# Kernel tuning notes

Measured on AMD Instinct MI355X. Metric: run time of the kernel, lower is better.

## Reference

```python
import jax, jax.numpy as jnp
import numpy as np
from jax import lax

DILATIONS = [1, 2, 4, 8, 16, 32, 64, 128, 256, 512]
KERNEL = 3
CH = 64
B, T = 8, 16384
L = len(DILATIONS)


def setup_inputs() -> dict:
    key = jax.random.key(0)
    ks = jax.random.split(key, 5)
    x = jax.random.normal(ks[0], (B, CH, T), dtype=jnp.float32)
    # gated conv: out_channels = 2*CH (tanh half | sigmoid half)
    weights_conv = jax.random.normal(ks[1], (L, 2 * CH, CH, KERNEL), dtype=jnp.float32) * 0.1
    biases_conv = jax.random.normal(ks[2], (L, 2 * CH), dtype=jnp.float32) * 0.1
    weights_out = jax.random.normal(ks[3], (L, CH, CH), dtype=jnp.float32) * 0.1
    biases_out = jax.random.normal(ks[4], (L, CH), dtype=jnp.float32) * 0.1
    return {
        "x": x,
        "weights_conv": weights_conv,
        "biases_conv": biases_conv,
        "weights_out": weights_out,
        "biases_out": biases_out,
    }


def _stack_forward(x, weights_conv, biases_conv, weights_out, biases_out):
    skips = []
    for i, d in enumerate(DILATIONS):
        h = x  # residual branch
        pad = (KERNEL - 1) * d  # causal left padding
        y = lax.conv_general_dilated(
            x, weights_conv[i],
            window_strides=(1,), padding=[(pad, 0)], rhs_dilation=(d,),
            dimension_numbers=("NCH", "OIH", "NCH"),
        ) + biases_conv[i][None, :, None]
        yt, ys = jnp.split(y, 2, axis=1)          # gated activation
        a = jnp.tanh(yt) * jax.nn.sigmoid(ys)      # (B, CH, T)
        skips.append(a)                            # skip = activation output
        if i < L - 1:  # last layer has use_output_transform=False
            out = jnp.einsum("oc,bct->bot", weights_out[i], a) + biases_out[i][None, :, None]
        else:
            out = a
        x = out + h  # residual add
    # pack (output, skips[0..L-1]) into one array of shape (L+1, B, CH, T)
    return jnp.concatenate([x[None], jnp.stack(skips, axis=0)], axis=0)


def reference(x, weights_conv, biases_conv, weights_out, biases_out):
    return _stack_forward(x, weights_conv, biases_conv, weights_out, biases_out)
```

## Files before the change

### kernel.cpp

```cpp
#include <hip/hip_runtime.h>
#include <hip/hip_bf16.h>


#define CH 64
#define TLEN 16384
#define NB 8
#define BN 128
#define NLAYER 10

#define WP   192
#define PSTR 194
#define ASTR 130

typedef __attribute__((ext_vector_type(4))) float f32x4;
typedef __attribute__((ext_vector_type(8))) short s16x8;
typedef __attribute__((ext_vector_type(4))) unsigned short u16x4;

__device__ __forceinline__ unsigned short f2bf(float f) {
    union { float f; unsigned u; } v; v.f = f;
    unsigned r = v.u + 0x7fffu + ((v.u >> 16) & 1u);
    return (unsigned short)(r >> 16);
}
__device__ __forceinline__ float bf2f(unsigned short u) {
    union { unsigned u; float f; } v; v.u = ((unsigned)u) << 16;
    return v.f;
}
__device__ __forceinline__ void gload_lds16(const void* g, void* l) {
    __builtin_amdgcn_global_load_lds(
        (const __attribute__((address_space(1))) unsigned int*)g,
        (__attribute__((address_space(3))) unsigned int*)l, 16, 0, 0);
}

#define NCONV (NLAYER * 4 * 2 * 6 * 64 * 8)
#define NOUT  (NLAYER * 4 * 2 * 64 * 8)

__global__ void pack_weights(const float* __restrict__ wconv,
                             const float* __restrict__ wout,
                             unsigned short* __restrict__ wcpk,
                             unsigned short* __restrict__ wopk)
{
    int idx = blockIdx.x * 256 + threadIdx.x;
    if (idx < NCONV) {
        int j = idx & 7, t = idx >> 3;
        int lane = t & 63; t >>= 6;
        int ks = t % 6;   t /= 6;
        int m  = t & 1;   t >>= 1;
        int wv = t & 3;   int l = t >> 2;
        int o  = (m * 4 + wv) * 16 + (lane & 15);
        int ck = ks * 32 + (lane >> 4) * 8 + j;
        int kk = ck >> 6, c = ck & 63;
        wcpk[idx] = f2bf(wconv[(((size_t)l * 128 + o) * CH + c) * 3 + (2 - kk)]);
    } else if (idx < NCONV + NOUT) {
        int id = idx - NCONV;
        int j = id & 7, t = id >> 3;
        int lane = t & 63; t >>= 6;
        int ks = t & 1;    t >>= 1;
        int wv = t & 3;    int l = t >> 2;
        int o  = wv * 16 + (lane & 15);
        int c  = ks * 32 + (lane >> 4) * 8 + j;
        wopk[id] = f2bf(wout[((size_t)l * CH + o) * CH + c]);
    }
}

__global__ __launch_bounds__(256, 2)
void wavenet_head(const float* __restrict__ x, unsigned short* __restrict__ xplane,
                  float* __restrict__ out,
                  const unsigned short* __restrict__ wcpk,
                  const unsigned short* __restrict__ wopk,
                  const float* __restrict__ bconv, const float* __restrict__ bout)
{
    __shared__ __align__(16) unsigned short pl[2][8 * PSTR * 8];
    __shared__ __align__(16) unsigned short as_[8 * ASTR * 8];

    const int tid  = threadIdx.x;
    const int lane = tid & 63;
    const int wv   = tid >> 6;
    const int hrow = lane & 15;
    const int kgrp = lane >> 4;
    const int b  = blockIdx.y;
    const int t0 = blockIdx.x * BN;
    const size_t xbase  = (size_t)b * CH * TLEN;
    const size_t planeF = (size_t)NB * CH * TLEN;

    if (tid < WP) {
        const int tt = t0 - 64 + tid;
        #pragma unroll
        for (int c8 = 0; c8 < 8; ++c8) {
            s16x8 pk = {0, 0, 0, 0, 0, 0, 0, 0};
            if (tt >= 0) {
                const float* p = x + xbase + (size_t)(c8 * 8) * TLEN + tt;
                #pragma unroll
                for (int j = 0; j < 8; ++j) pk[j] = (short)f2bf(p[(size_t)j * TLEN]);
            }
            *reinterpret_cast<s16x8*>(&pl[0][(size_t)(c8 * PSTR + tid) * 8]) = pk;
        }
    }
    __syncthreads();

    int cur = 0;
    for (int l = 0; l < 5; ++l) {
        const int dil = 1 << l;
        unsigned short* plc = pl[cur];
        unsigned short* pln = pl[cur ^ 1];

        s16x8 wa[2][6];
        {
            const unsigned short* basew = wcpk + ((size_t)(l * 4 + wv) * 768 + lane) * 8;
            #pragma unroll
            for (int m = 0; m < 2; ++m)
                #pragma unroll
                for (int ks = 0; ks < 6; ++ks)
                    wa[m][ks] = *reinterpret_cast<const s16x8*>(basew + (size_t)(m * 6 + ks) * 512);
        }
        const float* Bc = bconv + (size_t)l * 128;
        float bt[4], bs[4];
        #pragma unroll
        for (int r = 0; r < 4; ++r) {
            bt[r] = Bc[wv * 16 + kgrp * 4 + r];
            bs[r] = Bc[64 + wv * 16 + kgrp * 4 + r];
        }
        s16x8 wa2[2];
        {
            const unsigned short* b2 = wopk + ((size_t)(l * 4 + wv) * 128 + lane) * 8;
            wa2[0] = *reinterpret_cast<const s16x8*>(b2);
            wa2[1] = *reinterpret_cast<const s16x8*>(b2 + 512);
        }
        const float* Bo = bout + (size_t)l * CH;
        float bo[4];
        #pragma unroll
        for (int r = 0; r < 4; ++r) bo[r] = Bo[wv * 16 + kgrp * 4 + r];

        f32x4 accT[12], accS[12];
        #pragma unroll
        for (int nt = 0; nt < 12; ++nt) {
            accT[nt] = (f32x4){0.f, 0.f, 0.f, 0.f};
            accS[nt] = (f32x4){0.f, 0.f, 0.f, 0.f};
        }
        #pragma unroll
        for (int nt = 0; nt < 12; ++nt) {
            #pragma unroll
            for (int ks = 0; ks < 6; ++ks) {
                const int kb = ks * 4 + kgrp;
                const int kk = kb >> 3, c8i = kb & 7;
                int q = nt * 16 + hrow - kk * dil;
                if (q < 0) q = 0;
                const s16x8 bf = *reinterpret_cast<const s16x8*>(&plc[(size_t)(c8i * PSTR + q) * 8]);
                accT[nt] = __builtin_amdgcn_mfma_f32_16x16x32_bf16(wa[0][ks], bf, accT[nt], 0, 0, 0);
                accS[nt] = __builtin_amdgcn_mfma_f32_16x16x32_bf16(wa[1][ks], bf, accS[nt], 0, 0, 0);
            }
        }

        float* skipl = out + (size_t)(1 + l) * planeF + xbase;
        const int o0 = wv * 16 + kgrp * 4;

        #pragma unroll
        for (int nt = 0; nt < 8; ++nt) {
            #pragma unroll
            for (int r = 0; r < 4; ++r) {
                const float yt = accT[nt][r] + bt[r];
                const float ys = accS[nt][r] + bs[r];
                const float th = 2.f * __builtin_amdgcn_rcpf(1.f + __expf(-2.f * yt)) - 1.f;
                const float sg = __builtin_amdgcn_rcpf(1.f + __expf(-ys));
                const float av = th * sg;
                const int c = wv * 16 + kgrp * 4 + r;
                const int p = nt * 16 + hrow;
                if (nt >= 4) skipl[(size_t)c * TLEN + t0 + p - 64] = av;
                as_[(size_t)((c >> 3) * ASTR + p) * 8 + (c & 7)] = f2bf(av);
            }
        }
        __syncthreads();
        #pragma unroll
        for (int nt = 0; nt < 8; ++nt) {
            f32x4 a2 = (f32x4){0.f, 0.f, 0.f, 0.f};
            const int p = nt * 16 + hrow;
            #pragma unroll
            for (int ks2 = 0; ks2 < 2; ++ks2) {
                const s16x8 bf = *reinterpret_cast<const s16x8*>(
                    &as_[(size_t)((ks2 * 4 + kgrp) * ASTR + p) * 8]);
                a2 = __builtin_amdgcn_mfma_f32_16x16x32_bf16(wa2[ks2], bf, a2, 0, 0, 0);
            }
            const int tt = t0 - 64 + p;
            const u16x4 rv = *reinterpret_cast<const u16x4*>(
                &plc[(size_t)((o0 >> 3) * PSTR + p) * 8 + (o0 & 7)]);
            if (l == 4) {
                if (nt >= 4) {
                    u16x4 ov;
                    #pragma unroll
                    for (int r = 0; r < 4; ++r) ov[r] = f2bf(a2[r] + bo[r] + bf2f(rv[r]));
                    *reinterpret_cast<u16x4*>(&xplane[xbase + (size_t)tt * CH + o0]) = ov;
                }
            } else {
                u16x4 ov;
                #pragma unroll
                for (int r = 0; r < 4; ++r)
                    ov[r] = (tt >= 0) ? f2bf(a2[r] + bo[r] + bf2f(rv[r])) : (unsigned short)0;
                *reinterpret_cast<u16x4*>(&pln[(size_t)((o0 >> 3) * PSTR + p) * 8 + (o0 & 7)]) = ov;
            }
        }
        __syncthreads();
        #pragma unroll
        for (int nt = 8; nt < 12; ++nt) {
            #pragma unroll
            for (int r = 0; r < 4; ++r) {
                const float yt = accT[nt][r] + bt[r];
                const float ys = accS[nt][r] + bs[r];
                const float th = 2.f * __builtin_amdgcn_rcpf(1.f + __expf(-2.f * yt)) - 1.f;
                const float sg = __builtin_amdgcn_rcpf(1.f + __expf(-ys));
                const float av = th * sg;
                const int c = wv * 16 + kgrp * 4 + r;
                const int p = nt * 16 + hrow;
                skipl[(size_t)c * TLEN + t0 + p - 64] = av;
                as_[(size_t)((c >> 3) * ASTR + p - 128) * 8 + (c & 7)] = f2bf(av);
            }
        }
        __syncthreads();
        #pragma unroll
        for (int nt = 8; nt < 12; ++nt) {
            f32x4 a2 = (f32x4){0.f, 0.f, 0.f, 0.f};
            const int p = nt * 16 + hrow;
            #pragma unroll
            for (int ks2 = 0; ks2 < 2; ++ks2) {
                const s16x8 bf = *reinterpret_cast<const s16x8*>(
                    &as_[(size_t)((ks2 * 4 + kgrp) * ASTR + p - 128) * 8]);
                a2 = __builtin_amdgcn_mfma_f32_16x16x32_bf16(wa2[ks2], bf, a2, 0, 0, 0);
            }
            const int tt = t0 - 64 + p;
            const u16x4 rv = *reinterpret_cast<const u16x4*>(
                &plc[(size_t)((o0 >> 3) * PSTR + p) * 8 + (o0 & 7)]);
            if (l == 4) {
                u16x4 ov;
                #pragma unroll
                for (int r = 0; r < 4; ++r) ov[r] = f2bf(a2[r] + bo[r] + bf2f(rv[r]));
                *reinterpret_cast<u16x4*>(&xplane[xbase + (size_t)tt * CH + o0]) = ov;
            } else {
                u16x4 ov;
                #pragma unroll
                for (int r = 0; r < 4; ++r) ov[r] = f2bf(a2[r] + bo[r] + bf2f(rv[r]));
                *reinterpret_cast<u16x4*>(&pln[(size_t)((o0 >> 3) * PSTR + p) * 8 + (o0 & 7)]) = ov;
            }
        }
        __syncthreads();

        cur ^= 1;
    }
}

template<int SM, bool LAST>
__global__ __launch_bounds__(256, 3)
void wavenet_layer(const void* __restrict__ xin_, void* __restrict__ xout_,
                   float* __restrict__ skip,
                   const unsigned short* __restrict__ wcpk,
                   const unsigned short* __restrict__ wopk,
                   const float* __restrict__ bconv, const float* __restrict__ bout,
                   int layer, int dil)
{
    extern __shared__ __align__(16) unsigned short xs[];
    unsigned short* as_ = xs;

    const int tid  = threadIdx.x;
    const int lane = tid & 63;
    const int wv   = tid >> 6;
    const int hrow = lane & 15;
    const int kgrp = lane >> 4;
    const int b  = blockIdx.y;
    const int t0 = blockIdx.x * BN;
    const int NW = BN + 2 * dil;
    const size_t xbase = (size_t)b * CH * TLEN;

    if (SM == 1) {
        const unsigned short* xin = (const unsigned short*)xin_;
        const int cnt_n = (NW + 63) >> 6;
        if (t0 >= 2 * dil) {
            for (int ch = wv; ch < 8 * cnt_n; ch += 4) {
                const int c8 = ch / cnt_n;
                const int n0 = (ch % cnt_n) * 64;
                const int rem = NW - n0;
                const unsigned short* src =
                    xin + xbase + (size_t)(t0 - 2 * dil + n0 + lane) * CH + c8 * 8;
                unsigned short* dst = &xs[(size_t)(c8 * NW + n0) * 8];
                if (rem >= 64) gload_lds16(src, dst);
                else if (lane < rem) gload_lds16(src, dst);
            }
        } else {
            for (int ch = wv; ch < 8 * cnt_n; ch += 4) {
                const int c8 = ch / cnt_n;
                const int n0 = (ch % cnt_n) * 64;
                if (n0 + lane < NW) {
                    const int tg = t0 - 2 * dil + n0 + lane;
                    s16x8 pk = {0, 0, 0, 0, 0, 0, 0, 0};
                    if (tg >= 0)
                        pk = *reinterpret_cast<const s16x8*>(xin + xbase + (size_t)tg * CH + c8 * 8);
                    *reinterpret_cast<s16x8*>(&xs[(size_t)(c8 * NW + n0 + lane) * 8]) = pk;
                }
            }
        }
    } else {
        const unsigned short* xin = (const unsigned short*)xin_;
        if (t0 >= 2 * dil) {
            for (int ch = wv; ch < 48; ch += 4) {
                const int kk = ch >> 4, c8 = (ch >> 1) & 7, n0 = (ch & 1) * 64;
                const unsigned short* src =
                    xin + xbase + (size_t)(t0 + n0 + lane - kk * dil) * CH + c8 * 8;
                unsigned short* dst = &xs[(size_t)((kk * 8 + c8) * BN + n0) * 8];
                gload_lds16(src, dst);
            }
        } else {
            for (int ch = wv; ch < 48; ch += 4) {
                const int kk = ch >> 4, c8 = (ch >> 1) & 7, n0 = (ch & 1) * 64;
                const int tg = t0 + n0 + lane - kk * dil;
                s16x8 pk = {0, 0, 0, 0, 0, 0, 0, 0};
                if (tg >= 0)
                    pk = *reinterpret_cast<const s16x8*>(xin + xbase + (size_t)tg * CH + c8 * 8);
                *reinterpret_cast<s16x8*>(&xs[(size_t)((kk * 8 + c8) * BN + n0 + lane) * 8]) = pk;
            }
        }
    }

    s16x8 wa[2][6];
    {
        const unsigned short* base = wcpk + ((size_t)(layer * 4 + wv) * 768 + lane) * 8;
        #pragma unroll
        for (int m = 0; m < 2; ++m)
            #pragma unroll
            for (int ks = 0; ks < 6; ++ks)
                wa[m][ks] = *reinterpret_cast<const s16x8*>(base + (size_t)(m * 6 + ks) * 512);
    }
    const float* Bc = bconv + (size_t)layer * 128;
    float bt[4], bs[4];
    #pragma unroll
    for (int r = 0; r < 4; ++r) {
        bt[r] = Bc[wv * 16 + kgrp * 4 + r];
        bs[r] = Bc[64 + wv * 16 + kgrp * 4 + r];
    }

    __syncthreads();

    f32x4 accT[8], accS[8];
    #pragma unroll
    for (int nt = 0; nt < 8; ++nt) {
        accT[nt] = (f32x4){0.f, 0.f, 0.f, 0.f};
        accS[nt] = (f32x4){0.f, 0.f, 0.f, 0.f};
    }
    #pragma unroll
    for (int nt = 0; nt < 8; ++nt) {
        #pragma unroll
        for (int ks = 0; ks < 6; ++ks) {
            const int kb = ks * 4 + kgrp;
            const unsigned short* bp;
            if (SM == 2) {
                bp = &xs[(size_t)(kb * BN + nt * 16 + hrow) * 8];
            } else {
                const int kk = kb >> 3, c8i = kb & 7;
                bp = &xs[(size_t)(c8i * NW + nt * 16 + hrow + (2 - kk) * dil) * 8];
            }
            const s16x8 bf = *reinterpret_cast<const s16x8*>(bp);
            accT[nt] = __builtin_amdgcn_mfma_f32_16x16x32_bf16(wa[0][ks], bf, accT[nt], 0, 0, 0);
            accS[nt] = __builtin_amdgcn_mfma_f32_16x16x32_bf16(wa[1][ks], bf, accS[nt], 0, 0, 0);
        }
    }

    if (!LAST) __syncthreads();

    #pragma unroll
    for (int nt = 0; nt < 8; ++nt) {
        #pragma unroll
        for (int r = 0; r < 4; ++r) {
            const float yt = accT[nt][r] + bt[r];
            const float ys = accS[nt][r] + bs[r];
            const float th = 2.f * __builtin_amdgcn_rcpf(1.f + __expf(-2.f * yt)) - 1.f;
            const float sg = __builtin_amdgcn_rcpf(1.f + __expf(-ys));
            const float av = th * sg;
            const int c = wv * 16 + kgrp * 4 + r;
            const int n = nt * 16 + hrow;
            skip[xbase + (size_t)c * TLEN + t0 + n] = av;
            if (LAST) {
                const float res = bf2f(xs[(size_t)((c >> 3) * BN + n) * 8 + (c & 7)]);
                ((float*)xout_)[xbase + (size_t)c * TLEN + t0 + n] = av + res;
            } else {
                as_[(size_t)((c >> 3) * BN + n) * 8 + (c & 7)] = f2bf(av);
            }
        }
    }

    if (LAST) return;

    __syncthreads();

    const unsigned short* b2 = wopk + ((size_t)(layer * 4 + wv) * 128 + lane) * 8;
    s16x8 wa2[2];
    wa2[0] = *reinterpret_cast<const s16x8*>(b2);
    wa2[1] = *reinterpret_cast<const s16x8*>(b2 + 512);
    const float* Bo = bout + (size_t)layer * CH;
    float bo[4];
    #pragma unroll
    for (int r = 0; r < 4; ++r) bo[r] = Bo[wv * 16 + kgrp * 4 + r];

    const int o0 = wv * 16 + kgrp * 4;
    unsigned short* xout = (unsigned short*)xout_;

    #pragma unroll
    for (int nt = 0; nt < 8; ++nt) {
        f32x4 acc = (f32x4){0.f, 0.f, 0.f, 0.f};
        #pragma unroll
        for (int ks = 0; ks < 2; ++ks) {
            const s16x8 bf = *reinterpret_cast<const s16x8*>(
                &as_[(size_t)((ks * 4 + kgrp) * BN + nt * 16 + hrow) * 8]);
            acc = __builtin_amdgcn_mfma_f32_16x16x32_bf16(wa2[ks], bf, acc, 0, 0, 0);
        }
        const int n = nt * 16 + hrow;
        const u16x4 rv = *reinterpret_cast<const u16x4*>(
            (const unsigned short*)xin_ + xbase + (size_t)(t0 + n) * CH + o0);
        u16x4 ov;
        #pragma unroll
        for (int r = 0; r < 4; ++r) ov[r] = f2bf(acc[r] + bo[r] + bf2f(rv[r]));
        *reinterpret_cast<u16x4*>(&xout[xbase + (size_t)(t0 + n) * CH + o0]) = ov;
    }
}

extern "C" void kernel_launch(void* const* d_in, const int* in_sizes, int n_in,
                              void* d_out, int out_size, void* d_ws, size_t ws_size,
                              hipStream_t stream)
{
    const float* x  = (const float*)d_in[0];
    const float* wc = (const float*)d_in[1];
    const float* bc = (const float*)d_in[2];
    const float* wo = (const float*)d_in[3];
    const float* bo = (const float*)d_in[4];
    float* out = (float*)d_out;
    const size_t planeF  = (size_t)NB * CH * TLEN;
    const size_t planeBy = planeF * sizeof(unsigned short);

    unsigned short* P0 = (unsigned short*)d_ws;
    unsigned short* P1 = (unsigned short*)((char*)d_ws + planeBy);
    unsigned short* wcpk = (unsigned short*)((char*)d_ws + 2 * planeBy);
    unsigned short* wopk = wcpk + NCONV;

    pack_weights<<<(NCONV + NOUT) / 256, 256, 0, stream>>>(wc, wo, wcpk, wopk);

    dim3 grid(TLEN / BN, NB), block(256);

    wavenet_head<<<grid, block, 0, stream>>>(x, P0, out, wcpk, wopk, bc, bo);

    wavenet_layer<1, false><<<grid, block, (size_t)(BN + 64) * 128, stream>>>(
        P0, P1, out + 6 * planeF, wcpk, wopk, bc, bo, 5, 32);
    wavenet_layer<1, false><<<grid, block, (size_t)(BN + 128) * 128, stream>>>(
        P1, P0, out + 7 * planeF, wcpk, wopk, bc, bo, 6, 64);
    wavenet_layer<2, false><<<grid, block, 24 * BN * 8 * 2, stream>>>(
        P0, P1, out + 8 * planeF, wcpk, wopk, bc, bo, 7, 128);
    wavenet_layer<2, false><<<grid, block, 24 * BN * 8 * 2, stream>>>(
        P1, P0, out + 9 * planeF, wcpk, wopk, bc, bo, 8, 256);
    wavenet_layer<2, true><<<grid, block, 24 * BN * 8 * 2, stream>>>(
        P0, out, out + 10 * planeF, wcpk, wopk, bc, bo, 9, 512);
}
```

Measured before the change: 248.2 us.

## Double block to 512 threads, split time tiles across wave halves

```diff
diff --git a/kernel.cpp b/kernel.cpp
--- a/kernel.cpp
+++ b/kernel.cpp
@@ -10,7 +10,7 @@
 
 #define WP   192
 #define PSTR 194
-#define ASTR 130
+#define ASTR 194
 
 typedef __attribute__((ext_vector_type(4))) float f32x4;
 typedef __attribute__((ext_vector_type(8))) short s16x8;
@@ -62,7 +62,7 @@
     }
 }
 
-__global__ __launch_bounds__(256, 2)
+__global__ __launch_bounds__(512, 4)
 void wavenet_head(const float* __restrict__ x, unsigned short* __restrict__ xplane,
                   float* __restrict__ out,
                   const unsigned short* __restrict__ wcpk,
@@ -74,7 +74,9 @@
 
     const int tid  = threadIdx.x;
     const int lane = tid & 63;
-    const int wv   = tid >> 6;
+    const int wv8  = tid >> 6;
+    const int mw   = wv8 & 3;
+    const int nh   = wv8 >> 2;
     const int hrow = lane & 15;
     const int kgrp = lane >> 4;
     const int b  = blockIdx.y;
@@ -82,18 +84,18 @@
     const size_t xbase  = (size_t)b * CH * TLEN;
     const size_t planeF = (size_t)NB * CH * TLEN;
 
-    if (tid < WP) {
-        const int tt = t0 - 64 + tid;
-        #pragma unroll
-        for (int c8 = 0; c8 < 8; ++c8) {
-            s16x8 pk = {0, 0, 0, 0, 0, 0, 0, 0};
-            if (tt >= 0) {
-                const float* p = x + xbase + (size_t)(c8 * 8) * TLEN + tt;
-                #pragma unroll
-                for (int j = 0; j < 8; ++j) pk[j] = (short)f2bf(p[(size_t)j * TLEN]);
-            }
-            *reinterpret_cast<s16x8*>(&pl[0][(size_t)(c8 * PSTR + tid) * 8]) = pk;
-        }
+    #pragma unroll
+    for (int it = 0; it < 3; ++it) {
+        const int q  = it * 512 + tid;
+        const int c8 = q / WP, p = q % WP;
+        const int tt = t0 - 64 + p;
+        s16x8 pk = {0, 0, 0, 0, 0, 0, 0, 0};
+        if (tt >= 0) {
+            const float* pp = x + xbase + (size_t)(c8 * 8) * TLEN + tt;
+            #pragma unroll
+            for (int j = 0; j < 8; ++j) pk[j] = (short)f2bf(pp[(size_t)j * TLEN]);
+        }
+        *reinterpret_cast<s16x8*>(&pl[0][(size_t)(c8 * PSTR + p) * 8]) = pk;
     }
     __syncthreads();
 
@@ -103,76 +105,84 @@
         unsigned short* plc = pl[cur];
         unsigned short* pln = pl[cur ^ 1];
 
-        s16x8 wa[2][6];
+        s16x8 w0[6], w1[6];
         {
-            const unsigned short* basew = wcpk + ((size_t)(l * 4 + wv) * 768 + lane) * 8;
-            #pragma unroll
-            for (int m = 0; m < 2; ++m)
-                #pragma unroll
-                for (int ks = 0; ks < 6; ++ks)
-                    wa[m][ks] = *reinterpret_cast<const s16x8*>(basew + (size_t)(m * 6 + ks) * 512);
+            const unsigned short* basew = wcpk + ((size_t)(l * 4 + mw) * 768 + lane) * 8;
+            #pragma unroll
+            for (int ks = 0; ks < 6; ++ks) {
+                w0[ks] = *reinterpret_cast<const s16x8*>(basew + (size_t)ks * 512);
+                w1[ks] = *reinterpret_cast<const s16x8*>(basew + (size_t)(6 + ks) * 512);
+            }
         }
         const float* Bc = bconv + (size_t)l * 128;
         float bt[4], bs[4];
         #pragma unroll
         for (int r = 0; r < 4; ++r) {
-            bt[r] = Bc[wv * 16 + kgrp * 4 + r];
-            bs[r] = Bc[64 + wv * 16 + kgrp * 4 + r];
-        }
+            bt[r] = Bc[mw * 16 + kgrp * 4 + r];
+            bs[r] = Bc[64 + mw * 16 + kgrp * 4 + r];
+        }
+        float* skipl = out + (size_t)(1 + l) * planeF + xbase;
+
+        #pragma unroll 1
+        for (int hf = 0; hf < 2; ++hf) {
+            f32x4 accT[3], accS[3];
+            #pragma unroll
+            for (int i3 = 0; i3 < 3; ++i3) {
+                accT[i3] = (f32x4){0.f, 0.f, 0.f, 0.f};
+                accS[i3] = (f32x4){0.f, 0.f, 0.f, 0.f};
+            }
+            #pragma unroll
+            for (int i3 = 0; i3 < 3; ++i3) {
+                const int nt = nh * 6 + hf * 3 + i3;
+                const int p  = nt * 16 + hrow;
+                #pragma unroll
+                for (int ks = 0; ks < 6; ++ks) {
+                    const int kb = ks * 4 + kgrp;
+                    const int kk = kb >> 3, c8i = kb & 7;
+                    int q = p - kk * dil;
+                    if (q < 0) q = 0;
+                    const s16x8 bf = *reinterpret_cast<const s16x8*>(
+                        &plc[(size_t)(c8i * PSTR + q) * 8]);
+                    accT[i3] = __builtin_amdgcn_mfma_f32_16x16x32_bf16(w0[ks], bf, accT[i3], 0, 0, 0);
+                    accS[i3] = __builtin_amdgcn_mfma_f32_16x16x32_bf16(w1[ks], bf, accS[i3], 0, 0, 0);
+                }
+            }
+            #pragma unroll
+            for (int i3 = 0; i3 < 3; ++i3) {
+                const int nt = nh * 6 + hf * 3 + i3;
+                const int p  = nt * 16 + hrow;
+                #pragma unroll
+                for (int r = 0; r < 4; ++r) {
+                    const float yt = accT[i3][r] + bt[r];
+                    const float ys = accS[i3][r] + bs[r];
+                    const float th = 2.f * __builtin_amdgcn_rcpf(1.f + __expf(-2.f * yt)) - 1.f;
+                    const float sg = __builtin_amdgcn_rcpf(1.f + __expf(-ys));
+                    const float av = th * sg;
+                    const int c = mw * 16 + kgrp * 4 + r;
+                    if (nt >= 4) skipl[(size_t)c * TLEN + t0 + p - 64] = av;
+                    as_[(size_t)((c >> 3) * ASTR + p) * 8 + (c & 7)] = f2bf(av);
+                }
+            }
+        }
+        __syncthreads();
+
         s16x8 wa2[2];
         {
-            const unsigned short* b2 = wopk + ((size_t)(l * 4 + wv) * 128 + lane) * 8;
+            const unsigned short* b2 = wopk + ((size_t)(l * 4 + mw) * 128 + lane) * 8;
             wa2[0] = *reinterpret_cast<const s16x8*>(b2);
             wa2[1] = *reinterpret_cast<const s16x8*>(b2 + 512);
         }
         const float* Bo = bout + (size_t)l * CH;
         float bo[4];
         #pragma unroll
-        for (int r = 0; r < 4; ++r) bo[r] = Bo[wv * 16 + kgrp * 4 + r];
-
-        f32x4 accT[12], accS[12];
-        #pragma unroll
-        for (int nt = 0; nt < 12; ++nt) {
-            accT[nt] = (f32x4){0.f, 0.f, 0.f, 0.f};
-            accS[nt] = (f32x4){0.f, 0.f, 0.f, 0.f};
-        }
-        #pragma unroll
-        for (int nt = 0; nt < 12; ++nt) {
-            #pragma unroll
-            for (int ks = 0; ks < 6; ++ks) {
-                const int kb = ks * 4 + kgrp;
-                const int kk = kb >> 3, c8i = kb & 7;
-                int q = nt * 16 + hrow - kk * dil;
-                if (q < 0) q = 0;
-                const s16x8 bf = *reinterpret_cast<const s16x8*>(&plc[(size_t)(c8i * PSTR + q) * 8]);
-                accT[nt] = __builtin_amdgcn_mfma_f32_16x16x32_bf16(wa[0][ks], bf, accT[nt], 0, 0, 0);
-                accS[nt] = __builtin_amdgcn_mfma_f32_16x16x32_bf16(wa[1][ks], bf, accS[nt], 0, 0, 0);
-            }
-        }
-
-        float* skipl = out + (size_t)(1 + l) * planeF + xbase;
-        const int o0 = wv * 16 + kgrp * 4;
-
-        #pragma unroll
-        for (int nt = 0; nt < 8; ++nt) {
-            #pragma unroll
-            for (int r = 0; r < 4; ++r) {
-                const float yt = accT[nt][r] + bt[r];
-                const float ys = accS[nt][r] + bs[r];
-                const float th = 2.f * __builtin_amdgcn_rcpf(1.f + __expf(-2.f * yt)) - 1.f;
-                const float sg = __builtin_amdgcn_rcpf(1.f + __expf(-ys));
-                const float av = th * sg;
-                const int c = wv * 16 + kgrp * 4 + r;
-                const int p = nt * 16 + hrow;
-                if (nt >= 4) skipl[(size_t)c * TLEN + t0 + p - 64] = av;
-                as_[(size_t)((c >> 3) * ASTR + p) * 8 + (c & 7)] = f2bf(av);
-            }
-        }
-        __syncthreads();
-        #pragma unroll
-        for (int nt = 0; nt < 8; ++nt) {
+        for (int r = 0; r < 4; ++r) bo[r] = Bo[mw * 16 + kgrp * 4 + r];
+        const int o0 = mw * 16 + kgrp * 4;
+
+        #pragma unroll
+        for (int i = 0; i < 6; ++i) {
+            const int nt = nh * 6 + i;
+            const int p  = nt * 16 + hrow;
             f32x4 a2 = (f32x4){0.f, 0.f, 0.f, 0.f};
-            const int p = nt * 16 + hrow;
             #pragma unroll
             for (int ks2 = 0; ks2 < 2; ++ks2) {
                 const s16x8 bf = *reinterpret_cast<const s16x8*>(
@@ -198,55 +208,13 @@
             }
         }
         __syncthreads();
-        #pragma unroll
-        for (int nt = 8; nt < 12; ++nt) {
-            #pragma unroll
-            for (int r = 0; r < 4; ++r) {
-                const float yt = accT[nt][r] + bt[r];
-                const float ys = accS[nt][r] + bs[r];
-                const float th = 2.f * __builtin_amdgcn_rcpf(1.f + __expf(-2.f * yt)) - 1.f;
-                const float sg = __builtin_amdgcn_rcpf(1.f + __expf(-ys));
-                const float av = th * sg;
-                const int c = wv * 16 + kgrp * 4 + r;
-                const int p = nt * 16 + hrow;
-                skipl[(size_t)c * TLEN + t0 + p - 64] = av;
-                as_[(size_t)((c >> 3) * ASTR + p - 128) * 8 + (c & 7)] = f2bf(av);
-            }
-        }
-        __syncthreads();
-        #pragma unroll
-        for (int nt = 8; nt < 12; ++nt) {
-            f32x4 a2 = (f32x4){0.f, 0.f, 0.f, 0.f};
-            const int p = nt * 16 + hrow;
-            #pragma unroll
-            for (int ks2 = 0; ks2 < 2; ++ks2) {
-                const s16x8 bf = *reinterpret_cast<const s16x8*>(
-                    &as_[(size_t)((ks2 * 4 + kgrp) * ASTR + p - 128) * 8]);
-                a2 = __builtin_amdgcn_mfma_f32_16x16x32_bf16(wa2[ks2], bf, a2, 0, 0, 0);
-            }
-            const int tt = t0 - 64 + p;
-            const u16x4 rv = *reinterpret_cast<const u16x4*>(
-                &plc[(size_t)((o0 >> 3) * PSTR + p) * 8 + (o0 & 7)]);
-            if (l == 4) {
-                u16x4 ov;
-                #pragma unroll
-                for (int r = 0; r < 4; ++r) ov[r] = f2bf(a2[r] + bo[r] + bf2f(rv[r]));
-                *reinterpret_cast<u16x4*>(&xplane[xbase + (size_t)tt * CH + o0]) = ov;
-            } else {
-                u16x4 ov;
-                #pragma unroll
-                for (int r = 0; r < 4; ++r) ov[r] = f2bf(a2[r] + bo[r] + bf2f(rv[r]));
-                *reinterpret_cast<u16x4*>(&pln[(size_t)((o0 >> 3) * PSTR + p) * 8 + (o0 & 7)]) = ov;
-            }
-        }
-        __syncthreads();
 
         cur ^= 1;
     }
 }
 
 template<int SM, bool LAST>
-__global__ __launch_bounds__(256, 3)
+__global__ __launch_bounds__(512, 4)
 void wavenet_layer(const void* __restrict__ xin_, void* __restrict__ xout_,
                    float* __restrict__ skip,
                    const unsigned short* __restrict__ wcpk,
@@ -255,11 +223,13 @@
                    int layer, int dil)
 {
     extern __shared__ __align__(16) unsigned short xs[];
-    unsigned short* as_ = xs;
+    __shared__ __align__(16) unsigned short as_[8 * BN * 8];
 
     const int tid  = threadIdx.x;
     const int lane = tid & 63;
-    const int wv   = tid >> 6;
+    const int wv8  = tid >> 6;
+    const int mw   = wv8 & 3;
+    const int nh   = wv8 >> 2;
     const int hrow = lane & 15;
     const int kgrp = lane >> 4;
     const int b  = blockIdx.y;
@@ -271,7 +241,7 @@
         const unsigned short* xin = (const unsigned short*)xin_;
         const int cnt_n = (NW + 63) >> 6;
         if (t0 >= 2 * dil) {
-            for (int ch = wv; ch < 8 * cnt_n; ch += 4) {
+            for (int ch = wv8; ch < 8 * cnt_n; ch += 8) {
                 const int c8 = ch / cnt_n;
                 const int n0 = (ch % cnt_n) * 64;
                 const int rem = NW - n0;
@@ -282,7 +252,7 @@
                 else if (lane < rem) gload_lds16(src, dst);
             }
         } else {
-            for (int ch = wv; ch < 8 * cnt_n; ch += 4) {
+            for (int ch = wv8; ch < 8 * cnt_n; ch += 8) {
                 const int c8 = ch / cnt_n;
                 const int n0 = (ch % cnt_n) * 64;
                 if (n0 + lane < NW) {
@@ -297,7 +267,7 @@
     } else {
         const unsigned short* xin = (const unsigned short*)xin_;
         if (t0 >= 2 * dil) {
-            for (int ch = wv; ch < 48; ch += 4) {
+            for (int ch = wv8; ch < 48; ch += 8) {
                 const int kk = ch >> 4, c8 = (ch >> 1) & 7, n0 = (ch & 1) * 64;
                 const unsigned short* src =
                     xin + xbase + (size_t)(t0 + n0 + lane - kk * dil) * CH + c8 * 8;
@@ -305,7 +275,7 @@
                 gload_lds16(src, dst);
             }
         } else {
-            for (int ch = wv; ch < 48; ch += 4) {
+            for (int ch = wv8; ch < 48; ch += 8) {
                 const int kk = ch >> 4, c8 = (ch >> 1) & 7, n0 = (ch & 1) * 64;
                 const int tg = t0 + n0 + lane - kk * dil;
                 s16x8 pk = {0, 0, 0, 0, 0, 0, 0, 0};
@@ -316,68 +286,70 @@
         }
     }
 
-    s16x8 wa[2][6];
+    s16x8 w0[6], w1[6];
     {
-        const unsigned short* base = wcpk + ((size_t)(layer * 4 + wv) * 768 + lane) * 8;
-        #pragma unroll
-        for (int m = 0; m < 2; ++m)
-            #pragma unroll
-            for (int ks = 0; ks < 6; ++ks)
-                wa[m][ks] = *reinterpret_cast<const s16x8*>(base + (size_t)(m * 6 + ks) * 512);
+        const unsigned short* basew = wcpk + ((size_t)(layer * 4 + mw) * 768 + lane) * 8;
+        #pragma unroll
+        for (int ks = 0; ks < 6; ++ks) {
+            w0[ks] = *reinterpret_cast<const s16x8*>(basew + (size_t)ks * 512);
+            w1[ks] = *reinterpret_cast<const s16x8*>(basew + (size_t)(6 + ks) * 512);
+        }
     }
     const float* Bc = bconv + (size_t)layer * 128;
     float bt[4], bs[4];
     #pragma unroll
     for (int r = 0; r < 4; ++r) {
-        bt[r] = Bc[wv * 16 + kgrp * 4 + r];
-        bs[r] = Bc[64 + wv * 16 + kgrp * 4 + r];
+        bt[r] = Bc[mw * 16 + kgrp * 4 + r];
+        bs[r] = Bc[64 + mw * 16 + kgrp * 4 + r];
     }
 
     __syncthreads();
 
-    f32x4 accT[8], accS[8];
-    #pragma unroll
-    for (int nt = 0; nt < 8; ++nt) {
-        accT[nt] = (f32x4){0.f, 0.f, 0.f, 0.f};
-        accS[nt] = (f32x4){0.f, 0.f, 0.f, 0.f};
-    }
-    #pragma unroll
-    for (int nt = 0; nt < 8; ++nt) {
-        #pragma unroll
-        for (int ks = 0; ks < 6; ++ks) {
-            const int kb = ks * 4 + kgrp;
-            const unsigned short* bp;
-            if (SM == 2) {
-                bp = &xs[(size_t)(kb * BN + nt * 16 + hrow) * 8];
-            } else {
-                const int kk = kb >> 3, c8i = kb & 7;
-                bp = &xs[(size_t)(c8i * NW + nt * 16 + hrow + (2 - kk) * dil) * 8];
-            }
-            const s16x8 bf = *reinterpret_cast<const s16x8*>(bp);
-            accT[nt] = __builtin_amdgcn_mfma_f32_16x16x32_bf16(wa[0][ks], bf, accT[nt], 0, 0, 0);
-            accS[nt] = __builtin_amdgcn_mfma_f32_16x16x32_bf16(wa[1][ks], bf, accS[nt], 0, 0, 0);
-        }
-    }
-
-    if (!LAST) __syncthreads();
-
-    #pragma unroll
-    for (int nt = 0; nt < 8; ++nt) {
-        #pragma unroll
-        for (int r = 0; r < 4; ++r) {
-            const float yt = accT[nt][r] + bt[r];
-            const float ys = accS[nt][r] + bs[r];
-            const float th = 2.f * __builtin_amdgcn_rcpf(1.f + __expf(-2.f * yt)) - 1.f;
-            const float sg = __builtin_amdgcn_rcpf(1.f + __expf(-ys));
-            const float av = th * sg;
-            const int c = wv * 16 + kgrp * 4 + r;
-            const int n = nt * 16 + hrow;
-            skip[xbase + (size_t)c * TLEN + t0 + n] = av;
-            if (LAST) {
-                const float res = bf2f(xs[(size_t)((c >> 3) * BN + n) * 8 + (c & 7)]);
-                ((float*)xout_)[xbase + (size_t)c * TLEN + t0 + n] = av + res;
-            } else {
-                as_[(size_t)((c >> 3) * BN + n) * 8 + (c & 7)] = f2bf(av);
+    #pragma unroll 1
+    for (int hf = 0; hf < 2; ++hf) {
+        f32x4 accT[2], accS[2];
+        #pragma unroll
+        for (int i2 = 0; i2 < 2; ++i2) {
+            accT[i2] = (f32x4){0.f, 0.f, 0.f, 0.f};
+            accS[i2] = (f32x4){0.f, 0.f, 0.f, 0.f};
+        }
+        #pragma unroll
+        for (int i2 = 0; i2 < 2; ++i2) {
+            const int nt = nh * 4 + hf * 2 + i2;
+            #pragma unroll
+            for (int ks = 0; ks < 6; ++ks) {
+                const int kb = ks * 4 + kgrp;
+                const unsigned short* bp;
+                if (SM == 2) {
+                    bp = &xs[(size_t)(kb * BN + nt * 16 + hrow) * 8];
+                } else {
+                    const int kk = kb >> 3, c8i = kb & 7;
+                    bp = &xs[(size_t)(c8i * NW + nt * 16 + hrow + (2 - kk) * dil) * 8];
+                }
+                const s16x8 bf = *reinterpret_cast<const s16x8*>(bp);
+                accT[i2] = __builtin_amdgcn_mfma_f32_16x16x32_bf16(w0[ks], bf, accT[i2], 0, 0, 0);
+                accS[i2] = __builtin_amdgcn_mfma_f32_16x16x32_bf16(w1[ks], bf, accS[i2], 0, 0, 0);
+            }
+        }
+        #pragma unroll
+        for (int i2 = 0; i2 < 2; ++i2) {
+            const int nt = nh * 4 + hf * 2 + i2;
+            const int n  = nt * 16 + hrow;
+            #pragma unroll
+            for (int r = 0; r < 4; ++r) {
+                const float yt = accT[i2][r] + bt[r];
+                const float ys = accS[i2][r] + bs[r];
+                const float th = 2.f * __builtin_amdgcn_rcpf(1.f + __expf(-2.f * yt)) - 1.f;
+                const float sg = __builtin_amdgcn_rcpf(1.f + __expf(-ys));
+                const float av = th * sg;
+                const int c = mw * 16 + kgrp * 4 + r;
+                skip[xbase + (size_t)c * TLEN + t0 + n] = av;
+                if (LAST) {
+                    const float res = bf2f(xs[(size_t)((c >> 3) * BN + n) * 8 + (c & 7)]);
+                    ((float*)xout_)[xbase + (size_t)c * TLEN + t0 + n] = av + res;
+                } else {
+                    as_[(size_t)((c >> 3) * BN + n) * 8 + (c & 7)] = f2bf(av);
+                }
             }
         }
     }
@@ -386,28 +358,31 @@
 
     __syncthreads();
 
-    const unsigned short* b2 = wopk + ((size_t)(layer * 4 + wv) * 128 + lane) * 8;
     s16x8 wa2[2];
-    wa2[0] = *reinterpret_cast<const s16x8*>(b2);
-    wa2[1] = *reinterpret_cast<const s16x8*>(b2 + 512);
+    {
+        const unsigned short* b2 = wopk + ((size_t)(layer * 4 + mw) * 128 + lane) * 8;
+        wa2[0] = *reinterpret_cast<const s16x8*>(b2);
+        wa2[1] = *reinterpret_cast<const s16x8*>(b2 + 512);
+    }
     const float* Bo = bout + (size_t)layer * CH;
     float bo[4];
     #pragma unroll
-    for (int r = 0; r < 4; ++r) bo[r] = Bo[wv * 16 + kgrp * 4 + r];
-
-    const int o0 = wv * 16 + kgrp * 4;
+    for (int r = 0; r < 4; ++r) bo[r] = Bo[mw * 16 + kgrp * 4 + r];
+
+    const int o0 = mw * 16 + kgrp * 4;
     unsigned short* xout = (unsigned short*)xout_;
 
     #pragma unroll
-    for (int nt = 0; nt < 8; ++nt) {
+    for (int i = 0; i < 4; ++i) {
+        const int nt = nh * 4 + i;
+        const int n  = nt * 16 + hrow;
         f32x4 acc = (f32x4){0.f, 0.f, 0.f, 0.f};
         #pragma unroll
         for (int ks = 0; ks < 2; ++ks) {
             const s16x8 bf = *reinterpret_cast<const s16x8*>(
-                &as_[(size_t)((ks * 4 + kgrp) * BN + nt * 16 + hrow) * 8]);
+                &as_[(size_t)((ks * 4 + kgrp) * BN + n) * 8]);
             acc = __builtin_amdgcn_mfma_f32_16x16x32_bf16(wa2[ks], bf, acc, 0, 0, 0);
         }
-        const int n = nt * 16 + hrow;
         const u16x4 rv = *reinterpret_cast<const u16x4*>(
             (const unsigned short*)xin_ + xbase + (size_t)(t0 + n) * CH + o0);
         u16x4 ov;
@@ -437,7 +412,7 @@
 
     pack_weights<<<(NCONV + NOUT) / 256, 256, 0, stream>>>(wc, wo, wcpk, wopk);
 
-    dim3 grid(TLEN / BN, NB), block(256);
+    dim3 grid(TLEN / BN, NB), block(512);
 
     wavenet_head<<<grid, block, 0, stream>>>(x, P0, out, wcpk, wopk, bc, bo);
 
```

After: 267.2 us. 1.08x slower.

## Replace five-layer head kernel with three fused two-layer pair kernels

Applied to the files above, without the earlier changes.

```diff
diff --git a/kernel.cpp b/kernel.cpp
--- a/kernel.cpp
+++ b/kernel.cpp
@@ -7,10 +7,6 @@
 #define NB 8
 #define BN 128
 #define NLAYER 10
-
-#define WP   192
-#define PSTR 194
-#define ASTR 130
 
 typedef __attribute__((ext_vector_type(4))) float f32x4;
 typedef __attribute__((ext_vector_type(8))) short s16x8;
@@ -62,15 +58,26 @@
     }
 }
 
-__global__ __launch_bounds__(256, 2)
-void wavenet_head(const float* __restrict__ x, unsigned short* __restrict__ xplane,
+template<int I0, bool SRC_F32>
+__global__ __launch_bounds__(256, 4)
+void wavenet_pair(const void* __restrict__ xin_,
+                  unsigned short* __restrict__ xoutp,
                   float* __restrict__ out,
                   const unsigned short* __restrict__ wcpk,
                   const unsigned short* __restrict__ wopk,
-                  const float* __restrict__ bconv, const float* __restrict__ bout)
+                  const float* __restrict__ bconv,
+                  const float* __restrict__ bout)
 {
-    __shared__ __align__(16) unsigned short pl[2][8 * PSTR * 8];
-    __shared__ __align__(16) unsigned short as_[8 * ASTR * 8];
+    constexpr int d   = 1 << I0;
+    constexpr int D   = 2 * d;
+    constexpr int TD  = 2 * D;
+    constexpr int W1T = (128 + TD + 15) / 16;
+    constexpr int W1  = W1T * 16;
+    constexpr int WIN = W1 + 2 * d;
+
+    __shared__ __align__(16) unsigned short xs[WIN * 64];
+    __shared__ __align__(16) unsigned short ci[W1 * 64];
+    __shared__ __align__(16) unsigned short as2[64 * 64];
 
     const int tid  = threadIdx.x;
     const int lane = tid & 63;
@@ -81,167 +88,204 @@
     const int t0 = blockIdx.x * BN;
     const size_t xbase  = (size_t)b * CH * TLEN;
     const size_t planeF = (size_t)NB * CH * TLEN;
-
-    if (tid < WP) {
-        const int tt = t0 - 64 + tid;
+    const int o0 = wv * 16 + kgrp * 4;
+    const int lo = t0 - 6 * d;
+
+    if (SRC_F32) {
+        const float* x = (const float*)xin_;
         #pragma unroll
         for (int c8 = 0; c8 < 8; ++c8) {
-            s16x8 pk = {0, 0, 0, 0, 0, 0, 0, 0};
-            if (tt >= 0) {
-                const float* p = x + xbase + (size_t)(c8 * 8) * TLEN + tt;
-                #pragma unroll
-                for (int j = 0; j < 8; ++j) pk[j] = (short)f2bf(p[(size_t)j * TLEN]);
-            }
-            *reinterpret_cast<s16x8*>(&pl[0][(size_t)(c8 * PSTR + tid) * 8]) = pk;
-        }
-    }
+            for (int p = tid; p < WIN; p += 256) {
+                const int tt = lo + p;
+                s16x8 pk = {0, 0, 0, 0, 0, 0, 0, 0};
+                if (tt >= 0 && tt < TLEN) {
+                    const float* pp = x + xbase + (size_t)(c8 * 8) * TLEN + tt;
+                    #pragma unroll
+                    for (int j = 0; j < 8; ++j) pk[j] = (short)f2bf(pp[(size_t)j * TLEN]);
+                }
+                *reinterpret_cast<s16x8*>(&xs[(size_t)(c8 * WIN + p) * 8]) = pk;
+            }
+        }
+    } else {
+        const unsigned short* xb = (const unsigned short*)xin_ + xbase;
+        constexpr int cnt = (WIN + 63) / 64;
+        if (lo >= 0 && lo + WIN <= TLEN) {
+            for (int task = wv; task < 8 * cnt; task += 4) {
+                const int c8 = task / cnt, n0 = (task % cnt) * 64;
+                const int rem = WIN - n0;
+                const unsigned short* sp = xb + (size_t)(lo + n0 + lane) * CH + c8 * 8;
+                unsigned short* dp = &xs[(size_t)(c8 * WIN + n0) * 8];
+                if (rem >= 64) gload_lds16(sp, dp);
+                else if (lane < rem) gload_lds16(sp, dp);
+            }
+        } else {
+            for (int task = wv; task < 8 * cnt; task += 4) {
+                const int c8 = task / cnt, n0 = (task % cnt) * 64;
+                const int p = n0 + lane;
+                if (p < WIN) {
+                    const int tt = lo + p;
+                    s16x8 pk = {0, 0, 0, 0, 0, 0, 0, 0};
+                    if (tt >= 0 && tt < TLEN)
+                        pk = *reinterpret_cast<const s16x8*>(xb + (size_t)tt * CH + c8 * 8);
+                    *reinterpret_cast<s16x8*>(&xs[(size_t)(c8 * WIN + p) * 8]) = pk;
+                }
+            }
+        }
+    }
+
+    s16x8 w0[6], w1[6], wa2[2];
+    float bt[4], bs[4], bo[4];
+    auto loadw = [&](int L) {
+        const unsigned short* bw = wcpk + ((size_t)(L * 4 + wv) * 768 + lane) * 8;
+        #pragma unroll
+        for (int ks = 0; ks < 6; ++ks) {
+            w0[ks] = *reinterpret_cast<const s16x8*>(bw + (size_t)ks * 512);
+            w1[ks] = *reinterpret_cast<const s16x8*>(bw + (size_t)(6 + ks) * 512);
+        }
+        const unsigned short* b2 = wopk + ((size_t)(L * 4 + wv) * 128 + lane) * 8;
+        wa2[0] = *reinterpret_cast<const s16x8*>(b2);
+        wa2[1] = *reinterpret_cast<const s16x8*>(b2 + 512);
+        const float* Bc = bconv + (size_t)L * 128;
+        const float* Bo = bout + (size_t)L * CH;
+        #pragma unroll
+        for (int r = 0; r < 4; ++r) {
+            bt[r] = Bc[o0 + r];
+            bs[r] = Bc[64 + o0 + r];
+            bo[r] = Bo[o0 + r];
+        }
+    };
+
+    loadw(I0);
     __syncthreads();
 
-    int cur = 0;
-    for (int l = 0; l < 5; ++l) {
-        const int dil = 1 << l;
-        unsigned short* plc = pl[cur];
-        unsigned short* pln = pl[cur ^ 1];
-
-        s16x8 wa[2][6];
-        {
-            const unsigned short* basew = wcpk + ((size_t)(l * 4 + wv) * 768 + lane) * 8;
-            #pragma unroll
-            for (int m = 0; m < 2; ++m)
-                #pragma unroll
-                for (int ks = 0; ks < 6; ++ks)
-                    wa[m][ks] = *reinterpret_cast<const s16x8*>(basew + (size_t)(m * 6 + ks) * 512);
-        }
-        const float* Bc = bconv + (size_t)l * 128;
-        float bt[4], bs[4];
-        #pragma unroll
-        for (int r = 0; r < 4; ++r) {
-            bt[r] = Bc[wv * 16 + kgrp * 4 + r];
-            bs[r] = Bc[64 + wv * 16 + kgrp * 4 + r];
-        }
-        s16x8 wa2[2];
-        {
-            const unsigned short* b2 = wopk + ((size_t)(l * 4 + wv) * 128 + lane) * 8;
-            wa2[0] = *reinterpret_cast<const s16x8*>(b2);
-            wa2[1] = *reinterpret_cast<const s16x8*>(b2 + 512);
-        }
-        const float* Bo = bout + (size_t)l * CH;
-        float bo[4];
-        #pragma unroll
-        for (int r = 0; r < 4; ++r) bo[r] = Bo[wv * 16 + kgrp * 4 + r];
-
-        f32x4 accT[12], accS[12];
-        #pragma unroll
-        for (int nt = 0; nt < 12; ++nt) {
-            accT[nt] = (f32x4){0.f, 0.f, 0.f, 0.f};
-            accS[nt] = (f32x4){0.f, 0.f, 0.f, 0.f};
-        }
-        #pragma unroll
-        for (int nt = 0; nt < 12; ++nt) {
+    float* skipA = out + (size_t)(1 + I0) * planeF + xbase;
+    #pragma unroll 1
+    for (int c0 = 0; c0 < W1T; c0 += 3) {
+        f32x4 aT[3], aS[3];
+        #pragma unroll
+        for (int i3 = 0; i3 < 3; ++i3) {
+            aT[i3] = (f32x4){0.f, 0.f, 0.f, 0.f};
+            aS[i3] = (f32x4){0.f, 0.f, 0.f, 0.f};
+        }
+        #pragma unroll
+        for (int i3 = 0; i3 < 3; ++i3) {
+            const int q = (c0 + i3) * 16 + hrow;
             #pragma unroll
             for (int ks = 0; ks < 6; ++ks) {
                 const int kb = ks * 4 + kgrp;
                 const int kk = kb >> 3, c8i = kb & 7;
-                int q = nt * 16 + hrow - kk * dil;
-                if (q < 0) q = 0;
-                const s16x8 bf = *reinterpret_cast<const s16x8*>(&plc[(size_t)(c8i * PSTR + q) * 8]);
-                accT[nt] = __builtin_amdgcn_mfma_f32_16x16x32_bf16(wa[0][ks], bf, accT[nt], 0, 0, 0);
-                accS[nt] = __builtin_amdgcn_mfma_f32_16x16x32_bf16(wa[1][ks], bf, accS[nt], 0, 0, 0);
-            }
-        }
-
-        float* skipl = out + (size_t)(1 + l) * planeF + xbase;
-        const int o0 = wv * 16 + kgrp * 4;
-
-        #pragma unroll
-        for (int nt = 0; nt < 8; ++nt) {
+                const s16x8 bf = *reinterpret_cast<const s16x8*>(
+                    &xs[(size_t)(c8i * WIN + q + (2 - kk) * d) * 8]);
+                aT[i3] = __builtin_amdgcn_mfma_f32_16x16x32_bf16(w0[ks], bf, aT[i3], 0, 0, 0);
+                aS[i3] = __builtin_amdgcn_mfma_f32_16x16x32_bf16(w1[ks], bf, aS[i3], 0, 0, 0);
+            }
+        }
+        #pragma unroll
+        for (int i3 = 0; i3 < 3; ++i3) {
+            const int q = (c0 + i3) * 16 + hrow;
             #pragma unroll
             for (int r = 0; r < 4; ++r) {
-                const float yt = accT[nt][r] + bt[r];
-                const float ys = accS[nt][r] + bs[r];
+                const float yt = aT[i3][r] + bt[r];
+                const float ys = aS[i3][r] + bs[r];
                 const float th = 2.f * __builtin_amdgcn_rcpf(1.f + __expf(-2.f * yt)) - 1.f;
                 const float sg = __builtin_amdgcn_rcpf(1.f + __expf(-ys));
                 const float av = th * sg;
-                const int c = wv * 16 + kgrp * 4 + r;
-                const int p = nt * 16 + hrow;
-                if (nt >= 4) skipl[(size_t)c * TLEN + t0 + p - 64] = av;
-                as_[(size_t)((c >> 3) * ASTR + p) * 8 + (c & 7)] = f2bf(av);
+                const int c = o0 + r;
+                if (q >= TD && q < TD + 128)
+                    __builtin_nontemporal_store(av, &skipA[(size_t)c * TLEN + t0 + q - TD]);
+                ci[(size_t)((c >> 3) * W1 + q) * 8 + (c & 7)] = f2bf(av);
             }
         }
         __syncthreads();
-        #pragma unroll
-        for (int nt = 0; nt < 8; ++nt) {
-            f32x4 a2 = (f32x4){0.f, 0.f, 0.f, 0.f};
-            const int p = nt * 16 + hrow;
+        u16x4 stash[3];
+        #pragma unroll
+        for (int i3 = 0; i3 < 3; ++i3) {
+            const int q = (c0 + i3) * 16 + hrow;
+            f32x4 acc = (f32x4){0.f, 0.f, 0.f, 0.f};
             #pragma unroll
             for (int ks2 = 0; ks2 < 2; ++ks2) {
                 const s16x8 bf = *reinterpret_cast<const s16x8*>(
-                    &as_[(size_t)((ks2 * 4 + kgrp) * ASTR + p) * 8]);
-                a2 = __builtin_amdgcn_mfma_f32_16x16x32_bf16(wa2[ks2], bf, a2, 0, 0, 0);
-            }
-            const int tt = t0 - 64 + p;
+                    &ci[(size_t)((ks2 * 4 + kgrp) * W1 + q) * 8]);
+                acc = __builtin_amdgcn_mfma_f32_16x16x32_bf16(wa2[ks2], bf, acc, 0, 0, 0);
+            }
             const u16x4 rv = *reinterpret_cast<const u16x4*>(
-                &plc[(size_t)((o0 >> 3) * PSTR + p) * 8 + (o0 & 7)]);
-            if (l == 4) {
-                if (nt >= 4) {
-                    u16x4 ov;
-                    #pragma unroll
-                    for (int r = 0; r < 4; ++r) ov[r] = f2bf(a2[r] + bo[r] + bf2f(rv[r]));
-                    *reinterpret_cast<u16x4*>(&xplane[xbase + (size_t)tt * CH + o0]) = ov;
-                }
-            } else {
-                u16x4 ov;
-                #pragma unroll
-                for (int r = 0; r < 4; ++r)
-                    ov[r] = (tt >= 0) ? f2bf(a2[r] + bo[r] + bf2f(rv[r])) : (unsigned short)0;
-                *reinterpret_cast<u16x4*>(&pln[(size_t)((o0 >> 3) * PSTR + p) * 8 + (o0 & 7)]) = ov;
-            }
+                &xs[(size_t)((o0 >> 3) * WIN + q + 2 * d) * 8 + (o0 & 7)]);
+            u16x4 ov;
+            #pragma unroll
+            for (int r = 0; r < 4; ++r)
+                ov[r] = (t0 + q >= TD) ? f2bf(acc[r] + bo[r] + bf2f(rv[r]))
+                                       : (unsigned short)0;
+            stash[i3] = ov;
         }
         __syncthreads();
         #pragma unroll
-        for (int nt = 8; nt < 12; ++nt) {
+        for (int i3 = 0; i3 < 3; ++i3) {
+            const int q = (c0 + i3) * 16 + hrow;
+            *reinterpret_cast<u16x4*>(&ci[(size_t)((o0 >> 3) * W1 + q) * 8 + (o0 & 7)]) = stash[i3];
+        }
+    }
+    __syncthreads();
+
+    loadw(I0 + 1);
+    float* skipB = out + (size_t)(2 + I0) * planeF + xbase;
+    unsigned short* xo = xoutp + xbase;
+
+    #pragma unroll 1
+    for (int hf = 0; hf < 2; ++hf) {
+        f32x4 aT[4], aS[4];
+        #pragma unroll
+        for (int i4 = 0; i4 < 4; ++i4) {
+            aT[i4] = (f32x4){0.f, 0.f, 0.f, 0.f};
+            aS[i4] = (f32x4){0.f, 0.f, 0.f, 0.f};
+        }
+        #pragma unroll
+        for (int i4 = 0; i4 < 4; ++i4) {
+            const int n = (hf * 4 + i4) * 16 + hrow;
+            #pragma unroll
+            for (int ks = 0; ks < 6; ++ks) {
+                const int kb = ks * 4 + kgrp;
+                const int kk = kb >> 3, c8i = kb & 7;
+                const s16x8 bf = *reinterpret_cast<const s16x8*>(
+                    &ci[(size_t)(c8i * W1 + n + (2 - kk) * D) * 8]);
+                aT[i4] = __builtin_amdgcn_mfma_f32_16x16x32_bf16(w0[ks], bf, aT[i4], 0, 0, 0);
+                aS[i4] = __builtin_amdgcn_mfma_f32_16x16x32_bf16(w1[ks], bf, aS[i4], 0, 0, 0);
+            }
+        }
+        #pragma unroll
+        for (int i4 = 0; i4 < 4; ++i4) {
+            const int n = (hf * 4 + i4) * 16 + hrow;
             #pragma unroll
             for (int r = 0; r < 4; ++r) {
-                const float yt = accT[nt][r] + bt[r];
-                const float ys = accS[nt][r] + bs[r];
+                const float yt = aT[i4][r] + bt[r];
+                const float ys = aS[i4][r] + bs[r];
                 const float th = 2.f * __builtin_amdgcn_rcpf(1.f + __expf(-2.f * yt)) - 1.f;
                 const float sg = __builtin_amdgcn_rcpf(1.f + __expf(-ys));
                 const float av = th * sg;
-                const int c = wv * 16 + kgrp * 4 + r;
-                const int p = nt * 16 + hrow;
-                skipl[(size_t)c * TLEN + t0 + p - 64] = av;
-                as_[(size_t)((c >> 3) * ASTR + p - 128) * 8 + (c & 7)] = f2bf(av);
+                const int c = o0 + r;
+                __builtin_nontemporal_store(av, &skipB[(size_t)c * TLEN + t0 + n]);
+                as2[(size_t)((c >> 3) * 64 + (n - hf * 64)) * 8 + (c & 7)] = f2bf(av);
             }
         }
         __syncthreads();
         #pragma unroll
-        for (int nt = 8; nt < 12; ++nt) {
-            f32x4 a2 = (f32x4){0.f, 0.f, 0.f, 0.f};
-            const int p = nt * 16 + hrow;
+        for (int i4 = 0; i4 < 4; ++i4) {
+            const int n = (hf * 4 + i4) * 16 + hrow;
+            const int nl = n - hf * 64;
+            f32x4 acc = (f32x4){0.f, 0.f, 0.f, 0.f};
             #pragma unroll
             for (int ks2 = 0; ks2 < 2; ++ks2) {
                 const s16x8 bf = *reinterpret_cast<const s16x8*>(
-                    &as_[(size_t)((ks2 * 4 + kgrp) * ASTR + p - 128) * 8]);
-                a2 = __builtin_amdgcn_mfma_f32_16x16x32_bf16(wa2[ks2], bf, a2, 0, 0, 0);
-            }
-            const int tt = t0 - 64 + p;
+                    &as2[(size_t)((ks2 * 4 + kgrp) * 64 + nl) * 8]);
+                acc = __builtin_amdgcn_mfma_f32_16x16x32_bf16(wa2[ks2], bf, acc, 0, 0, 0);
+            }
             const u16x4 rv = *reinterpret_cast<const u16x4*>(
-                &plc[(size_t)((o0 >> 3) * PSTR + p) * 8 + (o0 & 7)]);
-            if (l == 4) {
-                u16x4 ov;
-                #pragma unroll
-                for (int r = 0; r < 4; ++r) ov[r] = f2bf(a2[r] + bo[r] + bf2f(rv[r]));
-                *reinterpret_cast<u16x4*>(&xplane[xbase + (size_t)tt * CH + o0]) = ov;
-            } else {
-                u16x4 ov;
-                #pragma unroll
-                for (int r = 0; r < 4; ++r) ov[r] = f2bf(a2[r] + bo[r] + bf2f(rv[r]));
-                *reinterpret_cast<u16x4*>(&pln[(size_t)((o0 >> 3) * PSTR + p) * 8 + (o0 & 7)]) = ov;
-            }
+                &ci[(size_t)((o0 >> 3) * W1 + n + TD) * 8 + (o0 & 7)]);
+            u16x4 ov;
+            #pragma unroll
+            for (int r = 0; r < 4; ++r) ov[r] = f2bf(acc[r] + bo[r] + bf2f(rv[r]));
+            *reinterpret_cast<u16x4*>(&xo[(size_t)(t0 + n) * CH + o0]) = ov;
         }
         __syncthreads();
-
-        cur ^= 1;
     }
 }
 
@@ -316,14 +360,14 @@
         }
     }
 
-    s16x8 wa[2][6];
+    s16x8 w0[6], w1[6];
     {
-        const unsigned short* base = wcpk + ((size_t)(layer * 4 + wv) * 768 + lane) * 8;
-        #pragma unroll
-        for (int m = 0; m < 2; ++m)
-            #pragma unroll
-            for (int ks = 0; ks < 6; ++ks)
-                wa[m][ks] = *reinterpret_cast<const s16x8*>(base + (size_t)(m * 6 + ks) * 512);
+        const unsigned short* basew = wcpk + ((size_t)(layer * 4 + wv) * 768 + lane) * 8;
+        #pragma unroll
+        for (int ks = 0; ks < 6; ++ks) {
+            w0[ks] = *reinterpret_cast<const s16x8*>(basew + (size_t)ks * 512);
+            w1[ks] = *reinterpret_cast<const s16x8*>(basew + (size_t)(6 + ks) * 512);
+        }
     }
     const float* Bc = bconv + (size_t)layer * 128;
     float bt[4], bs[4];
@@ -354,8 +398,8 @@
                 bp = &xs[(size_t)(c8i * NW + nt * 16 + hrow + (2 - kk) * dil) * 8];
             }
             const s16x8 bf = *reinterpret_cast<const s16x8*>(bp);
-            accT[nt] = __builtin_amdgcn_mfma_f32_16x16x32_bf16(wa[0][ks], bf, accT[nt], 0, 0, 0);
-            accS[nt] = __builtin_amdgcn_mfma_f32_16x16x32_bf16(wa[1][ks], bf, accS[nt], 0, 0, 0);
+            accT[nt] = __builtin_amdgcn_mfma_f32_16x16x32_bf16(w0[ks], bf, accT[nt], 0, 0, 0);
+            accS[nt] = __builtin_amdgcn_mfma_f32_16x16x32_bf16(w1[ks], bf, accS[nt], 0, 0, 0);
         }
     }
 
@@ -372,10 +416,11 @@
             const float av = th * sg;
             const int c = wv * 16 + kgrp * 4 + r;
             const int n = nt * 16 + hrow;
-            skip[xbase + (size_t)c * TLEN + t0 + n] = av;
+            __builtin_nontemporal_store(av, &skip[xbase + (size_t)c * TLEN + t0 + n]);
             if (LAST) {
                 const float res = bf2f(xs[(size_t)((c >> 3) * BN + n) * 8 + (c & 7)]);
-                ((float*)xout_)[xbase + (size_t)c * TLEN + t0 + n] = av + res;
+                __builtin_nontemporal_store(av + res,
+                    &((float*)xout_)[xbase + (size_t)c * TLEN + t0 + n]);
             } else {
                 as_[(size_t)((c >> 3) * BN + n) * 8 + (c & 7)] = f2bf(av);
             }
@@ -386,10 +431,12 @@
 
     __syncthreads();
 
-    const unsigned short* b2 = wopk + ((size_t)(layer * 4 + wv) * 128 + lane) * 8;
     s16x8 wa2[2];
-    wa2[0] = *reinterpret_cast<const s16x8*>(b2);
-    wa2[1] = *reinterpret_cast<const s16x8*>(b2 + 512);
+    {
+        const unsigned short* b2 = wopk + ((size_t)(layer * 4 + wv) * 128 + lane) * 8;
+        wa2[0] = *reinterpret_cast<const s16x8*>(b2);
+        wa2[1] = *reinterpret_cast<const s16x8*>(b2 + 512);
+    }
     const float* Bo = bout + (size_t)layer * CH;
     float bo[4];
     #pragma unroll
@@ -427,28 +474,27 @@
     const float* wo = (const float*)d_in[3];
     const float* bo = (const float*)d_in[4];
     float* out = (float*)d_out;
-    const size_t planeF  = (size_t)NB * CH * TLEN;
-    const size_t planeBy = planeF * sizeof(unsigned short);
-
-    unsigned short* P0 = (unsigned short*)d_ws;
-    unsigned short* P1 = (unsigned short*)((char*)d_ws + planeBy);
-    unsigned short* wcpk = (unsigned short*)((char*)d_ws + 2 * planeBy);
+    const size_t planeF = (size_t)NB * CH * TLEN;
+
+    unsigned short* PA = (unsigned short*)d_ws;
+    unsigned short* PB = PA + planeF;
+    unsigned short* wcpk = PB + planeF;
     unsigned short* wopk = wcpk + NCONV;
 
     pack_weights<<<(NCONV + NOUT) / 256, 256, 0, stream>>>(wc, wo, wcpk, wopk);
 
     dim3 grid(TLEN / BN, NB), block(256);
 
-    wavenet_head<<<grid, block, 0, stream>>>(x, P0, out, wcpk, wopk, bc, bo);
-
-    wavenet_layer<1, false><<<grid, block, (size_t)(BN + 64) * 128, stream>>>(
-        P0, P1, out + 6 * planeF, wcpk, wopk, bc, bo, 5, 32);
+    wavenet_pair<0, true ><<<grid, block, 0, stream>>>(x,  PA, out, wcpk, wopk, bc, bo);
+    wavenet_pair<2, false><<<grid, block, 0, stream>>>(PA, PB, out, wcpk, wopk, bc, bo);
+    wavenet_pair<4, false><<<grid, block, 0, stream>>>(PB, PA, out, wcpk, wopk, bc, bo);
+
     wavenet_layer<1, false><<<grid, block, (size_t)(BN + 128) * 128, stream>>>(
-        P1, P0, out + 7 * planeF, wcpk, wopk, bc, bo, 6, 64);
+        PA, PB, out + 7 * planeF, wcpk, wopk, bc, bo, 6, 64);
     wavenet_layer<2, false><<<grid, block, 24 * BN * 8 * 2, stream>>>(
-        P0, P1, out + 8 * planeF, wcpk, wopk, bc, bo, 7, 128);
+        PB, PA, out + 8 * planeF, wcpk, wopk, bc, bo, 7, 128);
     wavenet_layer<2, false><<<grid, block, 24 * BN * 8 * 2, stream>>>(
-        P1, P0, out + 9 * planeF, wcpk, wopk, bc, bo, 8, 256);
+        PA, PB, out + 9 * planeF, wcpk, wopk, bc, bo, 8, 256);
     wavenet_layer<2, true><<<grid, block, 24 * BN * 8 * 2, stream>>>(
-        P0, out, out + 10 * planeF, wcpk, wopk, bc, bo, 9, 512);
-}
+        PB, out, out + 10 * planeF, wcpk, wopk, bc, bo, 9, 512);
+}
```

Measured after the change: 233.8 us. -5.8%, faster.
